# Kernel optimization log

Measured on AMD Instinct MI355X. Metric: run time of the kernel, lower is better.

The kernel has to match this reference:

```python
import jax, jax.numpy as jnp
import numpy as np

D_MODEL = 2048
N_HEADS = 32
N_KV_HEADS = 8
D_K = D_MODEL // N_HEADS
HEADS_PER_GROUP = N_HEADS // N_KV_HEADS
B, S = 2, 2048


def setup_inputs() -> dict:
    key = jax.random.key(0)
    ks = jax.random.split(key, 12)
    scale = 1.0 / np.sqrt(D_MODEL)
    inp = {
        "q": jax.random.normal(ks[0], (B, S, D_MODEL), jnp.float32),
        "k": jax.random.normal(ks[1], (B, S, D_MODEL), jnp.float32),
        "v": jax.random.normal(ks[2], (B, S, D_MODEL), jnp.float32),
        # causal mask, broadcastable over [B, H, S, S]
        "mask": jnp.tril(jnp.ones((S, S), jnp.bool_))[None, None],
        # torch Linear convention: W [out, in], y = x @ W.T + b
        "Wq": jax.random.normal(ks[3], (D_MODEL, D_MODEL), jnp.float32) * scale,
        "bq": jax.random.normal(ks[4], (D_MODEL,), jnp.float32) * 0.01,
        "Wk": jax.random.normal(ks[5], (N_KV_HEADS * D_K, D_MODEL), jnp.float32) * scale,
        "bk": jax.random.normal(ks[6], (N_KV_HEADS * D_K,), jnp.float32) * 0.01,
        "Wv": jax.random.normal(ks[7], (N_KV_HEADS * D_K, D_MODEL), jnp.float32) * scale,
        "bv": jax.random.normal(ks[8], (N_KV_HEADS * D_K,), jnp.float32) * 0.01,
        "Wo": jax.random.normal(ks[9], (D_MODEL, D_MODEL), jnp.float32) * scale,
        "bo": jax.random.normal(ks[10], (D_MODEL,), jnp.float32) * 0.01,
    }
    return inp


def reference(q, k, v, mask, Wq, bq, Wk, bk, Wv, bv, Wo, bo):
    b, s, _ = q.shape
    # projections (torch Linear: x @ W.T + b)
    query = q @ Wq.T + bq                      # [B, S, D]
    key = k @ Wk.T + bk                        # [B, S, Kv*dk]
    value = v @ Wv.T + bv
    # [B, Kv, G, S, dk] for query (group heads per kv head instead of repeating K/V)
    query = query.reshape(b, s, N_KV_HEADS, HEADS_PER_GROUP, D_K).transpose(0, 2, 3, 1, 4)
    key = key.reshape(b, s, N_KV_HEADS, D_K).transpose(0, 2, 1, 3)      # [B, Kv, S, dk]
    value = value.reshape(b, s, N_KV_HEADS, D_K).transpose(0, 2, 1, 3)  # [B, Kv, S, dk]
    scores = jnp.einsum('bkgqd,bksd->bkgqs', query, key) / jnp.sqrt(jnp.float32(D_K))
    # mask is [1,1,S,S] broadcastable; add group axis
    scores = jnp.where(mask[:, :, None], scores, jnp.float32(-1e9))
    attn = jax.nn.softmax(scores, axis=-1)     # dropout p=0.0 -> identity
    out = jnp.einsum('bkgqs,bksd->bkgqd', attn, value)  # [B, Kv, G, S, dk]
    out = out.transpose(0, 3, 1, 2, 4).reshape(b, s, D_MODEL)
    return out @ Wo.T + bo
```

## Files before the change

### kernel.cpp

```cpp
#include <hip/hip_runtime.h>
#include <cstdint>

#define D_MODEL 2048
#define NKV 8
#define GQ 4
#define DK 64
#define B_ 2
#define S_ 2048
#define MS (B_*S_)
#define KVD (NKV*DK)

typedef unsigned short u16;
typedef __attribute__((ext_vector_type(8))) short bf16x8;
typedef __attribute__((ext_vector_type(4))) short bf16x4;
typedef __attribute__((ext_vector_type(4))) float f32x4;
typedef __attribute__((ext_vector_type(16))) float f32x16;
typedef __attribute__((ext_vector_type(4))) unsigned short u16x4;

__device__ __forceinline__ u16 f2bf(float f) {
    union { float f; uint32_t u; } x; x.f = f;
    uint32_t u = x.u;
    uint32_t r = (u + 0x7FFFu + ((u >> 16) & 1u)) >> 16;
    return (u16)r;
}
__device__ __forceinline__ float bf2f(u16 h) {
    union { uint32_t u; float f; } x; x.u = ((uint32_t)h) << 16;
    return x.f;
}

__device__ __forceinline__ void gload_lds16(const void* g, void* lds) {
    __builtin_amdgcn_global_load_lds(
        (const __attribute__((address_space(1))) void*)g,
        (__attribute__((address_space(3))) void*)lds, 16, 0, 0);
}

__device__ __forceinline__ bf16x8 cvt8(float4 a, float4 b) {
    union { unsigned u[4]; bf16x8 v; } r;
    asm("v_cvt_pk_bf16_f32 %0, %1, %2" : "=v"(r.u[0]) : "v"(a.x), "v"(a.y));
    asm("v_cvt_pk_bf16_f32 %0, %1, %2" : "=v"(r.u[1]) : "v"(a.z), "v"(a.w));
    asm("v_cvt_pk_bf16_f32 %0, %1, %2" : "=v"(r.u[2]) : "v"(b.x), "v"(b.y));
    asm("v_cvt_pk_bf16_f32 %0, %1, %2" : "=v"(r.u[3]) : "v"(b.z), "v"(b.w));
    return r.v;
}

__global__ __launch_bounds__(512, 2)
void gemm_qkv(const float* __restrict__ Aq, const float* __restrict__ Ak,
              const float* __restrict__ Av,
              const float* __restrict__ Wq, const float* __restrict__ Wk,
              const float* __restrict__ Wv,
              const float* __restrict__ bq, const float* __restrict__ bk,
              const float* __restrict__ bv,
              u16* __restrict__ Qp, u16* __restrict__ Kp, u16* __restrict__ Vt) {
    __shared__ __align__(16) u16 SA[2][256 * 64];
    __shared__ __align__(16) u16 SB[2][128 * 64];
    const int tid = threadIdx.x;
    const int lane = tid & 63;
    const int fr = lane & 15, fq = lane >> 4;
    const int wid = tid >> 6;
    const int wr = wid >> 1, wc = wid & 1;
    const int K = D_MODEL, NT = K / 64;

    const int bid = blockIdx.x;
    const int sw = (bid & 7) * 48 + (bid >> 3);
    const float* A; const float* Bw; const float* bias;
    int seg, by, bx;
    if (sw < 256)      { seg = 0; A = Aq; Bw = Wq; bias = bq; by = sw >> 4;        bx = sw & 15; }
    else if (sw < 320) { seg = 1; A = Ak; Bw = Wk; bias = bk; by = (sw - 256) >> 2; bx = (sw - 256) & 3; }
    else               { seg = 2; A = Av; Bw = Wv; bias = bv; by = (sw - 320) >> 2; bx = (sw - 320) & 3; }
    const int m0 = by * 256, n0 = bx * 128;

    float4 ra[4][2], rb[2][2];
    auto LOADA = [&](int t) {
        const int k0 = t << 6;
#pragma unroll
        for (int j = 0; j < 4; ++j) {
            int idx = tid + j * 512, row = idx >> 3, c = idx & 7;
            const float* p = A + (size_t)(m0 + row) * K + k0 + c * 8;
            ra[j][0] = *(const float4*)p;
            ra[j][1] = *(const float4*)(p + 4);
        }
    };
    auto LOADB = [&](int t) {
        const int k0 = t << 6;
#pragma unroll
        for (int j = 0; j < 2; ++j) {
            int idx = tid + j * 512, row = idx >> 3, c = idx & 7;
            const float* p = Bw + (size_t)(n0 + row) * K + k0 + c * 8;
            rb[j][0] = *(const float4*)p;
            rb[j][1] = *(const float4*)(p + 4);
        }
    };
    auto WRITE = [&](int q) {
#pragma unroll
        for (int j = 0; j < 4; ++j) {
            int idx = tid + j * 512, row = idx >> 3, c = idx & 7;
            *(bf16x8*)((char*)&SA[q][0] + row * 128 + ((c ^ (row & 7)) * 16)) = cvt8(ra[j][0], ra[j][1]);
        }
#pragma unroll
        for (int j = 0; j < 2; ++j) {
            int idx = tid + j * 512, row = idx >> 3, c = idx & 7;
            *(bf16x8*)((char*)&SB[q][0] + row * 128 + ((c ^ (row & 7)) * 16)) = cvt8(rb[j][0], rb[j][1]);
        }
    };

    f32x4 acc[4][4] = {};
    const int arow = wr * 64, brow = wc * 64;

    LOADA(0); LOADB(0);
    WRITE(0);
    LOADA(1); LOADB(1);
    asm volatile("s_waitcnt lgkmcnt(0)" ::: "memory");
    __builtin_amdgcn_s_barrier();

    for (int t = 0; t < NT; ++t) {
        const int q = t & 1;
        const char* sa = (const char*)&SA[q][0];
        const char* sb = (const char*)&SB[q][0];
#pragma unroll
        for (int kk = 0; kk < 2; ++kk) {
            const int cs = (((kk << 2) | fq) ^ (fr & 7)) * 16;
            bf16x8 af[4], bfr[4];
#pragma unroll
            for (int m = 0; m < 4; ++m)
                af[m] = *(const bf16x8*)(sa + (size_t)(arow + m * 16 + fr) * 128 + cs);
#pragma unroll
            for (int n = 0; n < 4; ++n)
                bfr[n] = *(const bf16x8*)(sb + (size_t)(brow + n * 16 + fr) * 128 + cs);
            __builtin_amdgcn_s_setprio(1);
#pragma unroll
            for (int m = 0; m < 4; ++m)
#pragma unroll
                for (int n = 0; n < 4; ++n)
                    acc[m][n] = __builtin_amdgcn_mfma_f32_16x16x32_bf16(af[m], bfr[n], acc[m][n], 0, 0, 0);
            __builtin_amdgcn_s_setprio(0);
        }
        asm volatile("s_barrier" ::: "memory");
        if (t + 1 < NT) {
            WRITE(q ^ 1);
            if (t + 2 < NT) { LOADA(t + 2); LOADB(t + 2); }
            asm volatile("s_waitcnt lgkmcnt(0)" ::: "memory");
            __builtin_amdgcn_s_barrier();
        }
    }

    float bvv[4];
#pragma unroll
    for (int n = 0; n < 4; ++n) bvv[n] = bias[n0 + brow + n * 16 + fr];
#pragma unroll
    for (int m = 0; m < 4; ++m) {
        int grow0 = m0 + wr * 64 + m * 16 + fq * 4;
#pragma unroll
        for (int n = 0; n < 4; ++n) {
            int gcol = n0 + brow + n * 16 + fr;
#pragma unroll
            for (int r = 0; r < 4; ++r) {
                float v = acc[m][n][r] + bvv[n];
                int grow = grow0 + r;
                if (seg == 0)      Qp[(size_t)grow * D_MODEL + gcol] = f2bf(v);
                else if (seg == 1) Kp[(size_t)grow * KVD + gcol] = f2bf(v);
                else {
                    int b = grow >> 11, s = grow & (S_ - 1);
                    Vt[((size_t)b * KVD + gcol) * S_ + s] = f2bf(v);
                }
            }
        }
    }
}

__global__ __launch_bounds__(512, 2)
void gemm_o(const u16* __restrict__ A, const float* __restrict__ Bw,
            const float* __restrict__ bias, float* __restrict__ Cout) {
    __shared__ __align__(16) u16 SA[2][256 * 64];
    __shared__ __align__(16) u16 SB[2][128 * 64];
    const int tid = threadIdx.x;
    const int lane = tid & 63;
    const int fr = lane & 15, fq = lane >> 4;
    const int wid = tid >> 6;
    const int wr = wid >> 1, wc = wid & 1;
    const int K = D_MODEL, N = D_MODEL, NT = K / 64;

    const int bid = blockIdx.x;
    const int sw = (bid & 7) * 32 + (bid >> 3);
    const int by = sw >> 4, bx = sw & 15;
    const int m0 = by * 256, n0 = bx * 128;

    auto GLOADA = [&](int t, int q) {
        const int k0 = t << 6;
#pragma unroll
        for (int j = 0; j < 4; ++j) {
            int idx = tid + j * 512, row = idx >> 3, c = idx & 7;
            gload_lds16(A + (size_t)(m0 + row) * K + k0 + ((c ^ (row & 7)) * 8),
                        &SA[q][(j * 512 + (tid >> 6) * 64) * 8]);
        }
    };
    float4 rb[2][2];
    auto LOADB = [&](int t) {
        const int k0 = t << 6;
#pragma unroll
        for (int j = 0; j < 2; ++j) {
            int idx = tid + j * 512, row = idx >> 3, c = idx & 7;
            const float* p = Bw + (size_t)(n0 + row) * K + k0 + c * 8;
            rb[j][0] = *(const float4*)p;
            rb[j][1] = *(const float4*)(p + 4);
        }
    };
    auto WRITEB = [&](int q) {
#pragma unroll
        for (int j = 0; j < 2; ++j) {
            int idx = tid + j * 512, row = idx >> 3, c = idx & 7;
            *(bf16x8*)((char*)&SB[q][0] + row * 128 + ((c ^ (row & 7)) * 16)) = cvt8(rb[j][0], rb[j][1]);
        }
    };

    f32x4 acc[4][4] = {};
    const int arow = wr * 64, brow = wc * 64;

    GLOADA(0, 0);
    asm volatile("" ::: "memory");
    LOADB(0);
    WRITEB(0);
    GLOADA(1, 1);
    asm volatile("" ::: "memory");
    LOADB(1);
    asm volatile("s_waitcnt lgkmcnt(0)" ::: "memory");
    __builtin_amdgcn_s_barrier();

    for (int t = 0; t < NT; ++t) {
        const int q = t & 1;
        const char* sa = (const char*)&SA[q][0];
        const char* sb = (const char*)&SB[q][0];
#pragma unroll
        for (int kk = 0; kk < 2; ++kk) {
            const int cs = (((kk << 2) | fq) ^ (fr & 7)) * 16;
            bf16x8 af[4], bfr[4];
#pragma unroll
            for (int m = 0; m < 4; ++m)
                af[m] = *(const bf16x8*)(sa + (size_t)(arow + m * 16 + fr) * 128 + cs);
#pragma unroll
            for (int n = 0; n < 4; ++n)
                bfr[n] = *(const bf16x8*)(sb + (size_t)(brow + n * 16 + fr) * 128 + cs);
            __builtin_amdgcn_s_setprio(1);
#pragma unroll
            for (int m = 0; m < 4; ++m)
#pragma unroll
                for (int n = 0; n < 4; ++n)
                    acc[m][n] = __builtin_amdgcn_mfma_f32_16x16x32_bf16(af[m], bfr[n], acc[m][n], 0, 0, 0);
            __builtin_amdgcn_s_setprio(0);
        }
        asm volatile("s_barrier" ::: "memory");
        if (t + 1 < NT) {
            asm volatile("s_waitcnt vmcnt(4)" ::: "memory");
            WRITEB(q ^ 1);
            if (t + 2 < NT) {
                GLOADA(t + 2, q);
                asm volatile("" ::: "memory");
                LOADB(t + 2);
            }
            asm volatile("s_waitcnt lgkmcnt(0)" ::: "memory");
            __builtin_amdgcn_s_barrier();
        }
    }

    float bvv[4];
#pragma unroll
    for (int n = 0; n < 4; ++n) bvv[n] = bias[n0 + brow + n * 16 + fr];
#pragma unroll
    for (int m = 0; m < 4; ++m) {
        int grow0 = m0 + wr * 64 + m * 16 + fq * 4;
#pragma unroll
        for (int n = 0; n < 4; ++n) {
            int gcol = n0 + brow + n * 16 + fr;
#pragma unroll
            for (int r = 0; r < 4; ++r)
                Cout[(size_t)(grow0 + r) * N + gcol] = acc[m][n][r] + bvv[n];
        }
    }
}

__global__ __launch_bounds__(256, 4)
void attn_fwd(const u16* __restrict__ Qp, const u16* __restrict__ Kp,
              const u16* __restrict__ Vt, u16* __restrict__ AO) {
    __shared__ __align__(16) u16 Klds[2][4096];
    __shared__ __align__(16) u16 Vlds[2][4096];
    const int bid = blockIdx.x;
    const int qblk = 15 - (bid >> 6);
    const int rest = bid & 63;
    const int b = rest >> 5;
    const int kv = (rest >> 2) & 7;
    const int g = rest & 3;
    const int tid = threadIdx.x, w = tid >> 6, l = tid & 63;
    const int q31 = l & 31, hi = l >> 5;
    const int h = kv * GQ + g;
    const int qw = qblk * 128 + w * 32;
    const int q0 = qw + q31;

    const u16* kbase = Kp + (size_t)(b * S_) * KVD + kv * DK;
    const u16* vbase = Vt + ((size_t)b * KVD + kv * DK) * S_;

    const float SCALE = 0.125f * 1.44269504f;
    bf16x8 qf[4];
    const u16* qp = Qp + ((size_t)(b * S_) + q0) * D_MODEL + h * DK;
#pragma unroll
    for (int ks = 0; ks < 4; ++ks) {
        bf16x8 t = *(const bf16x8*)(qp + ks * 16 + hi * 8);
#pragma unroll
        for (int j = 0; j < 8; ++j) t[j] = (short)f2bf(bf2f((u16)t[j]) * SCALE);
        qf[ks] = t;
    }

    const int nt = 2 * qblk + 2;
    const int bound = (qw + 31) >> 6;

    auto STAGE = [&](int t, int bufsel) {
#pragma unroll
        for (int r = 0; r < 2; ++r) {
            int idx = r * 256 + tid;
            int row = idx >> 3;
            int slotK = (idx & 7) ^ (row & 7);
            int jV = (idx & 7) ^ ((row >> 1) & 7);
            u16* kdst = &Klds[bufsel][(r * 256 + w * 64) * 8];
            u16* vdst = &Vlds[bufsel][(r * 256 + w * 64) * 8];
            gload_lds16(kbase + (size_t)(t * 64 + row) * KVD + slotK * 8, kdst);
            gload_lds16(vbase + (size_t)row * S_ + t * 64 + jV * 8, vdst);
        }
    };

    f32x16 o0 = {}, o1 = {};
    float m_run = -1e30f, l_run = 0.f;

    STAGE(0, 0);
    __syncthreads();
    int cur = 0;
    for (int t = 0; t < nt; ++t) {
        if (t + 1 < nt) STAGE(t + 1, cur ^ 1);
        if (t <= bound) {
            const u16* Kc = Klds[cur];
            const u16* Vc = Vlds[cur];
            const int base0 = t * 64, base1 = t * 64 + 32;
            const bool act1 = (base1 <= qw + 31);

            f32x16 s0 = {};
            {
                const int row = q31;
#pragma unroll
                for (int ks = 0; ks < 4; ++ks) {
                    bf16x8 kf = *(const bf16x8*)&Kc[row * 64 + ((((ks << 1) | hi)) ^ (row & 7)) * 8];
                    s0 = __builtin_amdgcn_mfma_f32_32x32x16_bf16(kf, qf[ks], s0, 0, 0, 0);
                }
            }
            f32x16 s1 = {};
            if (act1) {
                const int row = 32 + q31;
#pragma unroll
                for (int ks = 0; ks < 4; ++ks) {
                    bf16x8 kf = *(const bf16x8*)&Kc[row * 64 + ((((ks << 1) | hi)) ^ (row & 7)) * 8];
                    s1 = __builtin_amdgcn_mfma_f32_32x32x16_bf16(kf, qf[ks], s1, 0, 0, 0);
                }
            }
            if (base0 + 31 > qw) {
#pragma unroll
                for (int r = 0; r < 16; ++r) {
                    int koff = (r & 3) + 8 * (r >> 2) + 4 * hi;
                    s0[r] = (base0 + koff <= q0) ? s0[r] : -1e30f;
                }
            }
            if (act1 && (base1 + 31 > qw)) {
#pragma unroll
                for (int r = 0; r < 16; ++r) {
                    int koff = (r & 3) + 8 * (r >> 2) + 4 * hi;
                    s1[r] = (base1 + koff <= q0) ? s1[r] : -1e30f;
                }
            }
            float pm = s0[0];
#pragma unroll
            for (int r = 1; r < 16; ++r) pm = fmaxf(pm, s0[r]);
            if (act1) {
#pragma unroll
                for (int r = 0; r < 16; ++r) pm = fmaxf(pm, s1[r]);
            }
            pm = fmaxf(pm, __shfl_xor(pm, 32));
            if (__any(pm > m_run + 8.0f)) {
                float mn = fmaxf(m_run, pm);
                float sc = __builtin_amdgcn_exp2f(m_run - mn);
                m_run = mn; l_run *= sc;
#pragma unroll
                for (int r = 0; r < 16; ++r) { o0[r] *= sc; o1[r] *= sc; }
            }
            float psum = 0.f;
#pragma unroll
            for (int r = 0; r < 16; ++r) { float p = __builtin_amdgcn_exp2f(s0[r] - m_run); s0[r] = p; psum += p; }
            if (act1) {
#pragma unroll
                for (int r = 0; r < 16; ++r) { float p = __builtin_amdgcn_exp2f(s1[r] - m_run); s1[r] = p; psum += p; }
            }
            l_run += psum;
            unsigned W0[8], W1[8];
#pragma unroll
            for (int tt = 0; tt < 8; ++tt)
                asm("v_cvt_pk_bf16_f32 %0, %1, %2" : "=v"(W0[tt]) : "v"(s0[2 * tt]), "v"(s0[2 * tt + 1]));
            if (act1) {
#pragma unroll
                for (int tt = 0; tt < 8; ++tt)
                    asm("v_cvt_pk_bf16_f32 %0, %1, %2" : "=v"(W1[tt]) : "v"(s1[2 * tt]), "v"(s1[2 * tt + 1]));
            }
#pragma unroll
            for (int sl = 0; sl < 2; ++sl) {
                union { unsigned u[4]; bf16x8 v; } bw;
#pragma unroll
                for (int i = 0; i < 4; ++i) bw.u[i] = W0[sl * 4 + i];
#pragma unroll
                for (int half = 0; half < 2; ++half) {
                    const int row = half * 32 + q31;
                    union { bf16x4 h4[2]; bf16x8 v; } vf;
                    int sa = (sl * 4 + hi) ^ (row & 14);
                    int sb = (sl * 4 + 2 + hi) ^ (row & 14);
                    vf.h4[0] = *(const bf16x4*)&Vc[row * 64 + sa * 4];
                    vf.h4[1] = *(const bf16x4*)&Vc[row * 64 + sb * 4];
                    if (half == 0) o0 = __builtin_amdgcn_mfma_f32_32x32x16_bf16(vf.v, bw.v, o0, 0, 0, 0);
                    else           o1 = __builtin_amdgcn_mfma_f32_32x32x16_bf16(vf.v, bw.v, o1, 0, 0, 0);
                }
            }
            if (act1) {
#pragma unroll
                for (int sl = 2; sl < 4; ++sl) {
                    union { unsigned u[4]; bf16x8 v; } bw;
#pragma unroll
                    for (int i = 0; i < 4; ++i) bw.u[i] = W1[(sl - 2) * 4 + i];
#pragma unroll
                    for (int half = 0; half < 2; ++half) {
                        const int row = half * 32 + q31;
                        union { bf16x4 h4[2]; bf16x8 v; } vf;
                        int sa = (sl * 4 + hi) ^ (row & 14);
                        int sb = (sl * 4 + 2 + hi) ^ (row & 14);
                        vf.h4[0] = *(const bf16x4*)&Vc[row * 64 + sa * 4];
                        vf.h4[1] = *(const bf16x4*)&Vc[row * 64 + sb * 4];
                        if (half == 0) o0 = __builtin_amdgcn_mfma_f32_32x32x16_bf16(vf.v, bw.v, o0, 0, 0, 0);
                        else           o1 = __builtin_amdgcn_mfma_f32_32x32x16_bf16(vf.v, bw.v, o1, 0, 0, 0);
                    }
                }
            }
        }
        __syncthreads();
        cur ^= 1;
    }

    float lt = l_run + __shfl_xor(l_run, 32);
    float rl = 1.0f / lt;
    u16* op = AO + ((size_t)(b * S_) + q0) * D_MODEL + h * DK;
#pragma unroll
    for (int half = 0; half < 2; ++half) {
#pragma unroll
        for (int rr = 0; rr < 16; rr += 4) {
            u16x4 pk;
#pragma unroll
            for (int i = 0; i < 4; ++i)
                pk[i] = f2bf((half ? o1[rr + i] : o0[rr + i]) * rl);
            *(u16x4*)(op + half * 32 + (rr >> 2) * 8 + 4 * hi) = pk;
        }
    }
}

extern "C" void kernel_launch(void* const* d_in, const int* in_sizes, int n_in,
                              void* d_out, int out_size, void* d_ws, size_t ws_size,
                              hipStream_t stream) {
    const float* q  = (const float*)d_in[0];
    const float* k  = (const float*)d_in[1];
    const float* v  = (const float*)d_in[2];
    const float* Wq = (const float*)d_in[4];
    const float* bq = (const float*)d_in[5];
    const float* Wk = (const float*)d_in[6];
    const float* bk = (const float*)d_in[7];
    const float* Wv = (const float*)d_in[8];
    const float* bv = (const float*)d_in[9];
    const float* Wo = (const float*)d_in[10];
    const float* bo = (const float*)d_in[11];
    float* out = (float*)d_out;

    char* ws = (char*)d_ws;
    size_t off = 0;
    auto alloc = [&](size_t bytes) -> void* {
        void* p = ws + off;
        off += (bytes + 255) & ~(size_t)255;
        return p;
    };
    u16* Qp = (u16*)alloc((size_t)MS * D_MODEL * 2);
    u16* Kp = (u16*)alloc((size_t)MS * KVD * 2);
    u16* Vt = (u16*)alloc((size_t)MS * KVD * 2);
    u16* AO = (u16*)alloc((size_t)MS * D_MODEL * 2);

    gemm_qkv<<<384, 512, 0, stream>>>(q, k, v, Wq, Wk, Wv, bq, bk, bv, Qp, Kp, Vt);

    attn_fwd<<<16 * 64, 256, 0, stream>>>(Qp, Kp, Vt, AO);

    gemm_o<<<256, 512, 0, stream>>>(AO, Wo, bo, out);
}
```

Before: 239.7 us.

## Shrink QKV GEMM tile to 128x128 and restructure LDS double-buffer pipeline

The QKV projection GEMM moves from 256x128 tiles with 512 threads to 128x128 tiles with 256 threads, doubling the grid to 768 blocks for better CU coverage. The main loop is reordered so the next tile's LDS write happens before the MFMAs and the global prefetch is issued after them. This removes one barrier per iteration, and sched_barriers pin the ordering. Smaller tiles mean more global re-reads of the A and W operands, and the new schedule relies on the double buffer to avoid LDS read/write hazards.

```diff
diff --git a/kernel.cpp b/kernel.cpp
--- a/kernel.cpp
+++ b/kernel.cpp
@@ -43,7 +43,7 @@
     return r.v;
 }
 
-__global__ __launch_bounds__(512, 2)
+__global__ __launch_bounds__(256, 2)
 void gemm_qkv(const float* __restrict__ Aq, const float* __restrict__ Ak,
               const float* __restrict__ Av,
               const float* __restrict__ Wq, const float* __restrict__ Wk,
@@ -51,55 +51,52 @@
               const float* __restrict__ bq, const float* __restrict__ bk,
               const float* __restrict__ bv,
               u16* __restrict__ Qp, u16* __restrict__ Kp, u16* __restrict__ Vt) {
-    __shared__ __align__(16) u16 SA[2][256 * 64];
+    __shared__ __align__(16) u16 SA[2][128 * 64];
     __shared__ __align__(16) u16 SB[2][128 * 64];
     const int tid = threadIdx.x;
     const int lane = tid & 63;
     const int fr = lane & 15, fq = lane >> 4;
-    const int wid = tid >> 6;
-    const int wr = wid >> 1, wc = wid & 1;
+    const int w = tid >> 6;
+    const int wr = w >> 1, wc = w & 1;
     const int K = D_MODEL, NT = K / 64;
 
     const int bid = blockIdx.x;
-    const int sw = (bid & 7) * 48 + (bid >> 3);
+    const int sw = (bid & 7) * 96 + (bid >> 3);
     const float* A; const float* Bw; const float* bias;
     int seg, by, bx;
-    if (sw < 256)      { seg = 0; A = Aq; Bw = Wq; bias = bq; by = sw >> 4;        bx = sw & 15; }
-    else if (sw < 320) { seg = 1; A = Ak; Bw = Wk; bias = bk; by = (sw - 256) >> 2; bx = (sw - 256) & 3; }
-    else               { seg = 2; A = Av; Bw = Wv; bias = bv; by = (sw - 320) >> 2; bx = (sw - 320) & 3; }
-    const int m0 = by * 256, n0 = bx * 128;
-
-    float4 ra[4][2], rb[2][2];
+    if (sw < 512)      { seg = 0; A = Aq; Bw = Wq; bias = bq; by = sw >> 4;         bx = sw & 15; }
+    else if (sw < 640) { seg = 1; A = Ak; Bw = Wk; bias = bk; by = (sw - 512) >> 2; bx = (sw - 512) & 3; }
+    else               { seg = 2; A = Av; Bw = Wv; bias = bv; by = (sw - 640) >> 2; bx = (sw - 640) & 3; }
+    const int m0 = by * 128, n0 = bx * 128;
+
+    const int sr = tid >> 3, sc = tid & 7;
+    float4 ra[4][2], rb[4][2];
     auto LOADA = [&](int t) {
-        const int k0 = t << 6;
+        const float* p0 = A + (size_t)(m0 + sr) * K + (t << 6) + sc * 8;
 #pragma unroll
         for (int j = 0; j < 4; ++j) {
-            int idx = tid + j * 512, row = idx >> 3, c = idx & 7;
-            const float* p = A + (size_t)(m0 + row) * K + k0 + c * 8;
-            ra[j][0] = *(const float4*)p;
-            ra[j][1] = *(const float4*)(p + 4);
+            const float* p = p0 + (size_t)(j * 32) * K;
+            ra[j][0] = *(const float4*)p; ra[j][1] = *(const float4*)(p + 4);
         }
     };
     auto LOADB = [&](int t) {
-        const int k0 = t << 6;
-#pragma unroll
-        for (int j = 0; j < 2; ++j) {
-            int idx = tid + j * 512, row = idx >> 3, c = idx & 7;
-            const float* p = Bw + (size_t)(n0 + row) * K + k0 + c * 8;
-            rb[j][0] = *(const float4*)p;
-            rb[j][1] = *(const float4*)(p + 4);
+        const float* p0 = Bw + (size_t)(n0 + sr) * K + (t << 6) + sc * 8;
+#pragma unroll
+        for (int j = 0; j < 4; ++j) {
+            const float* p = p0 + (size_t)(j * 32) * K;
+            rb[j][0] = *(const float4*)p; rb[j][1] = *(const float4*)(p + 4);
         }
     };
     auto WRITE = [&](int q) {
 #pragma unroll
         for (int j = 0; j < 4; ++j) {
-            int idx = tid + j * 512, row = idx >> 3, c = idx & 7;
-            *(bf16x8*)((char*)&SA[q][0] + row * 128 + ((c ^ (row & 7)) * 16)) = cvt8(ra[j][0], ra[j][1]);
-        }
-#pragma unroll
-        for (int j = 0; j < 2; ++j) {
-            int idx = tid + j * 512, row = idx >> 3, c = idx & 7;
-            *(bf16x8*)((char*)&SB[q][0] + row * 128 + ((c ^ (row & 7)) * 16)) = cvt8(rb[j][0], rb[j][1]);
+            int row = j * 32 + sr;
+            *(bf16x8*)((char*)&SA[q][0] + row * 128 + ((sc ^ (row & 7)) * 16)) = cvt8(ra[j][0], ra[j][1]);
+        }
+#pragma unroll
+        for (int j = 0; j < 4; ++j) {
+            int row = j * 32 + sr;
+            *(bf16x8*)((char*)&SB[q][0] + row * 128 + ((sc ^ (row & 7)) * 16)) = cvt8(rb[j][0], rb[j][1]);
         }
     };
 
@@ -111,9 +108,11 @@
     LOADA(1); LOADB(1);
     asm volatile("s_waitcnt lgkmcnt(0)" ::: "memory");
     __builtin_amdgcn_s_barrier();
+    __builtin_amdgcn_sched_barrier(0);
 
     for (int t = 0; t < NT; ++t) {
         const int q = t & 1;
+        if (t + 1 < NT) WRITE(q ^ 1);
         const char* sa = (const char*)&SA[q][0];
         const char* sb = (const char*)&SB[q][0];
 #pragma unroll
@@ -134,12 +133,11 @@
                     acc[m][n] = __builtin_amdgcn_mfma_f32_16x16x32_bf16(af[m], bfr[n], acc[m][n], 0, 0, 0);
             __builtin_amdgcn_s_setprio(0);
         }
-        asm volatile("s_barrier" ::: "memory");
+        if (t + 2 < NT) { LOADA(t + 2); LOADB(t + 2); }
         if (t + 1 < NT) {
-            WRITE(q ^ 1);
-            if (t + 2 < NT) { LOADA(t + 2); LOADB(t + 2); }
             asm volatile("s_waitcnt lgkmcnt(0)" ::: "memory");
             __builtin_amdgcn_s_barrier();
+            __builtin_amdgcn_sched_barrier(0);
         }
     }
 
@@ -148,7 +146,7 @@
     for (int n = 0; n < 4; ++n) bvv[n] = bias[n0 + brow + n * 16 + fr];
 #pragma unroll
     for (int m = 0; m < 4; ++m) {
-        int grow0 = m0 + wr * 64 + m * 16 + fq * 4;
+        int grow0 = m0 + arow + m * 16 + fq * 4;
 #pragma unroll
         for (int n = 0; n < 4; ++n) {
             int gcol = n0 + brow + n * 16 + fr;
@@ -488,7 +486,7 @@
     u16* Vt = (u16*)alloc((size_t)MS * KVD * 2);
     u16* AO = (u16*)alloc((size_t)MS * D_MODEL * 2);
 
-    gemm_qkv<<<384, 512, 0, stream>>>(q, k, v, Wq, Wk, Wv, bq, bk, bv, Qp, Kp, Vt);
+    gemm_qkv<<<768, 256, 0, stream>>>(q, k, v, Wq, Wk, Wv, bq, bk, bv, Qp, Kp, Vt);
 
     attn_fwd<<<16 * 64, 256, 0, stream>>>(Qp, Kp, Vt, AO);
 
```

New measurement: 209.5 us. 12.6% less time.
